# Optimization experiments

Measured on AMD Instinct MI355X. Metric: run time of the kernel, lower is better.

Reference implementation:

```python
import math
import jax, jax.numpy as jnp
import numpy as np

LAMBDA_TV = 0.005
LAMBDA_WAV = 0.005
MAX_ITER = 15
LEVELS = 3
TV_ITERS = 5  # prox_tv called with num_iter=5 in forward
S2 = math.sqrt(2.0)


def _fft2c(x):
    # x: (B, 2, H, W) real/imag channels -> centered 2D FFT, same layout
    xc = x[:, 0] + 1j * x[:, 1]
    kc = jnp.fft.fftshift(
        jnp.fft.fft2(jnp.fft.ifftshift(xc, axes=(-2, -1)), norm='ortho'),
        axes=(-2, -1))
    return jnp.stack([kc.real, kc.imag], axis=1)


def _ifft2c(x):
    xc = x[:, 0] + 1j * x[:, 1]
    ic = jnp.fft.fftshift(
        jnp.fft.ifft2(jnp.fft.ifftshift(xc, axes=(-2, -1)), norm='ortho'),
        axes=(-2, -1))
    return jnp.stack([ic.real, ic.imag], axis=1)


def _grad(x):
    # x: (N, 1, H, W) -> forward differences, (N, 2, H, W); last row/col zero
    dx = jnp.pad(x[:, :, :, 1:] - x[:, :, :, :-1], ((0, 0), (0, 0), (0, 0), (0, 1)))
    dy = jnp.pad(x[:, :, 1:, :] - x[:, :, :-1, :], ((0, 0), (0, 0), (0, 1), (0, 0)))
    return jnp.concatenate([dx, dy], axis=1)


def _div(p):
    # adjoint of _grad with the exact boundary handling of the torch code
    px, py = p[:, 0:1], p[:, 1:2]
    div_x = jnp.concatenate(
        [px[:, :, :, 0:1], px[:, :, :, 1:-1] - px[:, :, :, :-2], -px[:, :, :, -2:-1]],
        axis=-1)
    div_y = jnp.concatenate(
        [py[:, :, 0:1, :], py[:, :, 1:-1, :] - py[:, :, :-2, :], -py[:, :, -2:-1, :]],
        axis=2)
    return div_x + div_y


def _prox_tv(x, lam):
    # Chambolle dual iteration, applied per channel (vectorized over B*C)
    B, C, H, W = x.shape
    xc = x.reshape(B * C, 1, H, W)
    tau = 0.25

    def body(p, _):
        g = _grad(xc - lam * _div(p))
        pn = p + tau * g
        nrm = jnp.sqrt(jnp.sum(pn * pn, axis=1, keepdims=True) + 1e-8)
        return pn / jnp.maximum(nrm, 1.0), None

    p0 = jnp.zeros((B * C, 2, H, W), x.dtype)
    p, _ = jax.lax.scan(body, p0, None, length=TV_ITERS)
    return (xc - lam * _div(p)).reshape(B, C, H, W)


def _dwt2(x):
    x_lo = (x[:, :, :, ::2] + x[:, :, :, 1::2]) / S2
    x_hi = (x[:, :, :, ::2] - x[:, :, :, 1::2]) / S2
    ll = (x_lo[:, :, ::2] + x_lo[:, :, 1::2]) / S2
    lh = (x_lo[:, :, ::2] - x_lo[:, :, 1::2]) / S2
    hl = (x_hi[:, :, ::2] + x_hi[:, :, 1::2]) / S2
    hh = (x_hi[:, :, ::2] - x_hi[:, :, 1::2]) / S2
    return ll, (lh, hl, hh)


def _interleave(even, odd, axis):
    s = jnp.stack([even, odd], axis=axis + 1)
    shp = list(even.shape)
    shp[axis] *= 2
    return s.reshape(shp)


def _idwt2(ll, lh, hl, hh):
    x_lo = _interleave((ll + lh) / S2, (ll - lh) / S2, axis=2)  # rows
    x_hi = _interleave((hl + hh) / S2, (hl - hh) / S2, axis=2)
    return _interleave((x_lo + x_hi) / S2, (x_lo - x_hi) / S2, axis=3)  # cols


def _soft(x, t):
    return jnp.sign(x) * jnp.maximum(jnp.abs(x) - t, 0.0)


def setup_inputs() -> dict:
    key = jax.random.key(0)
    k1, k2 = jax.random.split(key)
    B, H, W = 16, 320, 320
    y = jax.random.normal(k1, (B, 2, H, W), jnp.float32)
    mask = (jax.random.uniform(k2, (B, 1, H, W)) < 0.3).astype(jnp.float32)
    return {"y": y, "mask": mask}


def reference(y, mask):
    def step(carry, _):
        x, z, t = carry
        # projected gradient for data fidelity (step_size = 1.0)
        g = _ifft2c(mask * (mask * _fft2c(z) - y))
        z_step = z - g
        # TV prox
        x_tv = _prox_tv(z_step, LAMBDA_TV)
        # wavelet decomposition + soft-threshold of detail subbands
        cur = x_tv
        details = []
        for _lvl in range(LEVELS):
            cur, d = _dwt2(cur)
            details.append(tuple(_soft(c, LAMBDA_WAV) for c in d))
        x_new = cur
        for d in reversed(details):
            x_new = _idwt2(x_new, *d)
        # FISTA momentum
        t_new = (1.0 + jnp.sqrt(1.0 + 4.0 * t * t)) / 2.0
        z_new = x_new + (t - 1.0) / t_new * (x_new - x)
        return (x_new, z_new, t_new), None

    x0 = _ifft2c(y)
    (x, _, _), _ = jax.lax.scan(jax.checkpoint(step), (x0, x0, jnp.float32(1.0)),
                                None, length=MAX_ITER)
    return x
```

## Files before the change

### kernel.cpp

```cpp
#include <hip/hip_runtime.h>
#include <math.h>

constexpr int WID  = 320;
constexpr int HWc  = 320 * 320;
constexpr int NIMG = 16;
constexpr int NSL  = 32;
constexpr int NTOT = NIMG * 2 * HWc;
constexpr float LAM_TV  = 0.005f;
constexpr float LAM_WAV = 0.005f;

__device__ __forceinline__ float softt(float v) {
    float a = fmaxf(fabsf(v) - LAM_WAV, 0.f);
    return copysignf(a, v);
}

struct Tw { float tc, ts; float stc[6], sts[6]; };

template<int SGN>
__device__ __forceinline__ Tw make_tw(int lane) {
    Tw tw;
    __sincosf((float)SGN * 6.283185307179586f * (float)lane / 320.f, &tw.ts, &tw.tc);
#pragma unroll
    for (int s = 0; s < 6; s++) {
        int h = 32 >> s;
        int j = lane & (h - 1);
        float ang = (float)SGN * 3.14159265358979323f * (float)j / (float)h;
        __sincosf(ang, &tw.sts[s], &tw.stc[s]);
    }
    return tw;
}

template<int SGN>
__device__ __forceinline__ void fft320_core(const float (&vr)[5], const float (&vi)[5],
                                            float (&Cr)[5], float (&Ci)[5],
                                            const Tw& tw, int lane) {
    const float cw1 = 0.30901699437494745f, sw1 = 0.9510565162951535f;
    const float cw2 = -0.8090169943749475f, sw2 = 0.5877852522924731f;
    const float cwt[5] = {1.f, cw1, cw2, cw2, cw1};
    const float swt[5] = {0.f, sw1, sw2, -sw2, -sw1};
    Cr[0] = vr[0] + vr[1] + vr[2] + vr[3] + vr[4];
    Ci[0] = vi[0] + vi[1] + vi[2] + vi[3] + vi[4];
#pragma unroll
    for (int k = 1; k < 5; k++) {
        float ar = vr[0], ai = vi[0];
#pragma unroll
        for (int m = 1; m < 5; m++) {
            int j = (m * k) % 5;
            float wr_ = cwt[j], wi_ = (float)SGN * swt[j];
            ar += vr[m] * wr_ - vi[m] * wi_;
            ai += vr[m] * wi_ + vi[m] * wr_;
        }
        Cr[k] = ar; Ci[k] = ai;
    }
    float twr = 1.f, twi = 0.f;
#pragma unroll
    for (int k = 1; k < 5; k++) {
        float nr = twr * tw.tc - twi * tw.ts;
        twi = twr * tw.ts + twi * tw.tc;
        twr = nr;
        float r = Cr[k] * twr - Ci[k] * twi;
        Ci[k]   = Cr[k] * twi + Ci[k] * twr;
        Cr[k]   = r;
    }
#pragma unroll
    for (int s = 0; s < 6; s++) {
        int h = 32 >> s;
        bool up = (lane & h) != 0;
#pragma unroll
        for (int k = 0; k < 5; k++) {
            float orr = __shfl_xor(Cr[k], h);
            float oii = __shfl_xor(Ci[k], h);
            if (up) {
                float dr = orr - Cr[k], di = oii - Ci[k];
                Cr[k] = dr * tw.stc[s] - di * tw.sts[s];
                Ci[k] = dr * tw.sts[s] + di * tw.stc[s];
            } else {
                Cr[k] += orr;
                Ci[k] += oii;
            }
        }
    }
}

template<int SGN, int EPI>
__global__ __launch_bounds__(256) void fft_row(const float* __restrict__ in,
                                               float* __restrict__ out,
                                               const float* __restrict__ aux1,
                                               float* __restrict__ out2) {
    const int lane = threadIdx.x & 63;
    const int wv   = threadIdx.x >> 6;
    const int L    = blockIdx.x * 4 + wv;
    const int img  = L / 320;
    const int l    = L - img * 320;
    const float* pre = in + (size_t)img * 2 * HWc + (size_t)l * WID;
    const float* pim = pre + HWc;

    float vr[5], vi[5];
    const float sgn_in = (lane & 1) ? -1.f : 1.f;
#pragma unroll
    for (int m = 0; m < 5; m++) {
        int n = lane + 64 * m;
        vr[m] = sgn_in * pre[n];
        vi[m] = sgn_in * pim[n];
    }
    Tw tw = make_tw<SGN>(lane);
    float Cr[5], Ci[5];
    fft320_core<SGN>(vr, vi, Cr, Ci, tw, lane);

    const int k1 = (int)(__brev((unsigned)lane) >> 26);
    float* qre = out + (size_t)img * 2 * HWc + (size_t)l * WID;
    float* qim = qre + HWc;
    const float scale = 0.05590169943749474f;
#pragma unroll
    for (int k = 0; k < 5; k++) {
        int kout = 5 * k1 + k;
        float s2 = (kout & 1) ? -scale : scale;
        float re = s2 * Cr[k];
        float im = s2 * Ci[k];
        const int idxs = kout + l * WID;
        if (EPI == 2) {
            re = aux1[(size_t)img * 2 * HWc + idxs] - re;
            im = aux1[(size_t)img * 2 * HWc + HWc + idxs] - im;
        }
        qre[kout] = re;
        qim[kout] = im;
        if (EPI == 3) {
            out2[(size_t)img * 2 * HWc + idxs]       = re;
            out2[(size_t)img * 2 * HWc + HWc + idxs] = im;
        }
    }
}

constexpr int CB   = 8;
constexpr int CPAD = CB + 1;

template<int SGN>
__device__ __forceinline__ void fft_line_lds(float (*tile)[320][CPAD], int cl,
                                             int lane, const Tw& tw) {
    float vr[5], vi[5], Cr[5], Ci[5];
    const float sgn_in = (lane & 1) ? -1.f : 1.f;
#pragma unroll
    for (int m = 0; m < 5; m++) {
        int n = lane + 64 * m;
        vr[m] = sgn_in * tile[0][n][cl];
        vi[m] = sgn_in * tile[1][n][cl];
    }
    fft320_core<SGN>(vr, vi, Cr, Ci, tw, lane);
    const int k1 = (int)(__brev((unsigned)lane) >> 26);
    const float scale = 0.05590169943749474f;
#pragma unroll
    for (int k = 0; k < 5; k++) {
        int kout = 5 * k1 + k;
        float s2 = (kout & 1) ? -scale : scale;
        tile[0][kout][cl] = s2 * Cr[k];
        tile[1][kout][cl] = s2 * Ci[k];
    }
}

template<int MODE>
__global__ __launch_bounds__(512) void fft_col(const float* __restrict__ in,
                                               float* __restrict__ out,
                                               const float* __restrict__ y,
                                               const float* __restrict__ mask) {
    __shared__ float tile[2][320][CPAD];
    const int tid = threadIdx.x;
    const int bpi = WID / CB;
    const int img = blockIdx.x / bpi;
    const int c0  = (blockIdx.x - img * bpi) * CB;
    const size_t ibase = (size_t)img * 2 * HWc;
    constexpr int C4 = CB / 4;
    constexpr int NE = 320 * C4;

#pragma unroll
    for (int comp = 0; comp < 2; comp++) {
        const float* p = in + ibase + (size_t)comp * HWc + c0;
        for (int i = tid; i < NE; i += 512) {
            int row = i >> 1, cg = (i & 1) << 2;
            float4 v = *(const float4*)(p + row * WID + cg);
            float* t = &tile[comp][row][cg];
            t[0] = v.x; t[1] = v.y; t[2] = v.z; t[3] = v.w;
        }
    }
    __syncthreads();

    const int lane = tid & 63;
    const int wv   = tid >> 6;

    if (MODE == 1) {
        Tw twf = make_tw<-1>(lane);
        fft_line_lds<-1>(tile, wv, lane, twf);
        __syncthreads();
        const float* pm  = mask + (size_t)img * HWc + c0;
        const float* pyr = y + ibase + c0;
        const float* pyi = y + ibase + HWc + c0;
        for (int i = tid; i < NE; i += 512) {
            int row = i >> 1, cg = (i & 1) << 2;
            float4 m4 = *(const float4*)(pm  + row * WID + cg);
            float4 yr = *(const float4*)(pyr + row * WID + cg);
            float4 yi = *(const float4*)(pyi + row * WID + cg);
            float* tr = &tile[0][row][cg];
            float* ti = &tile[1][row][cg];
            tr[0] = m4.x * (m4.x * tr[0] - yr.x);
            tr[1] = m4.y * (m4.y * tr[1] - yr.y);
            tr[2] = m4.z * (m4.z * tr[2] - yr.z);
            tr[3] = m4.w * (m4.w * tr[3] - yr.w);
            ti[0] = m4.x * (m4.x * ti[0] - yi.x);
            ti[1] = m4.y * (m4.y * ti[1] - yi.y);
            ti[2] = m4.z * (m4.z * ti[2] - yi.z);
            ti[3] = m4.w * (m4.w * ti[3] - yi.w);
        }
        __syncthreads();
    }
    {
        Tw twi = make_tw<1>(lane);
        fft_line_lds<1>(tile, wv, lane, twi);
    }
    __syncthreads();
#pragma unroll
    for (int comp = 0; comp < 2; comp++) {
        float* p = out + ibase + (size_t)comp * HWc + c0;
        for (int i = tid; i < NE; i += 512) {
            int row = i >> 1, cg = (i & 1) << 2;
            const float* t = &tile[comp][row][cg];
            *(float4*)(p + row * WID + cg) = make_float4(t[0], t[1], t[2], t[3]);
        }
    }
}

constexpr int TIR = 16;
constexpr int TVR = TIR + 10;
constexpr int TIC = 48;
constexpr int TCOLS = 7;
constexpr int TROWS = WID / TIR;
constexpr int TPS = TROWS * TCOLS;

template<bool EDGE>
__device__ __forceinline__ void tv_core(const float* __restrict__ g, int gi0, int gj,
                                        float (&uf)[TIR]) {
    float z_[TVR], px_[TVR], py_[TVR];
    const bool colin = !EDGE || ((unsigned)gj < (unsigned)WID);
#pragma unroll
    for (int r = 0; r < TVR; r++) {
        int gi = gi0 + r;
        float v = 0.f;
        if (!EDGE) {
            v = g[gi * WID + gj];
        } else {
            bool in = colin && ((unsigned)gi < (unsigned)WID);
            if (in) v = g[gi * WID + gj];
        }
        z_[r] = v; px_[r] = 0.f; py_[r] = 0.f;
    }
    const bool gj_le0 = EDGE && (gj <= 0);
    const bool gj_hi  = EDGE && (gj >= WID - 1);
    const bool gx_on  = !EDGE || (gj < WID - 1);

#pragma clang loop unroll(disable)
    for (int it = 0; it < 5; it++) {
        float ucur, unext;
        {
            float pxm = __shfl_up(px_[0], 1);
            float divx, divy;
            if (!EDGE) {
                divx = px_[0] - pxm;
                divy = 0.f;
            } else {
                int gi = gi0;
                divx = gj_le0 ? px_[0] : (gj_hi ? -pxm : px_[0] - pxm);
                divy = (gi <= 0) ? py_[0] : ((gi >= WID - 1) ? -py_[0] : 0.f);
            }
            ucur = z_[0] - LAM_TV * (divx + divy);
        }
#pragma unroll
        for (int r = 0; r < TVR - 1; r++) {
            {
                float pxm = __shfl_up(px_[r + 1], 1);
                float divx, divy;
                if (!EDGE) {
                    divx = px_[r + 1] - pxm;
                    divy = py_[r + 1] - py_[r];
                } else {
                    int gi1 = gi0 + r + 1;
                    divx = gj_le0 ? px_[r + 1] : (gj_hi ? -pxm : px_[r + 1] - pxm);
                    divy = (gi1 <= 0) ? py_[r + 1]
                         : ((gi1 >= WID - 1) ? -py_[r] : py_[r + 1] - py_[r]);
                }
                unext = z_[r + 1] - LAM_TV * (divx + divy);
            }
            {
                float un = __shfl_down(ucur, 1);
                float gx, gy;
                if (!EDGE) {
                    gx = un - ucur;
                    gy = unext - ucur;
                } else {
                    int gi = gi0 + r;
                    gx = gx_on ? un - ucur : 0.f;
                    gy = (gi < WID - 1) ? unext - ucur : 0.f;
                }
                float px = fmaf(0.25f, gx, px_[r]);
                float py = fmaf(0.25f, gy, py_[r]);
                float n2 = fmaf(px, px, fmaf(py, py, 1e-8f));
                float inv = fminf(rsqrtf(n2), 1.f);
                px_[r] = px * inv;
                py_[r] = py * inv;
            }
            ucur = unext;
        }
        {
            float un = __shfl_down(ucur, 1);
            float gx = gx_on ? un - ucur : 0.f;
            float px = fmaf(0.25f, gx, px_[TVR - 1]);
            float py = py_[TVR - 1];
            float n2 = fmaf(px, px, fmaf(py, py, 1e-8f));
            float inv = fminf(rsqrtf(n2), 1.f);
            px_[TVR - 1] = px * inv;
            py_[TVR - 1] = py * inv;
        }
    }
#pragma unroll
    for (int r = 5; r < TVR - 5; r++) {
        float pxm = __shfl_up(px_[r], 1);
        float divx, divy;
        if (!EDGE) {
            divx = px_[r] - pxm;
            divy = py_[r] - py_[r - 1];
        } else {
            int gi = gi0 + r;
            divx = gj_le0 ? px_[r] : (gj_hi ? -pxm : px_[r] - pxm);
            divy = (gi <= 0) ? py_[r]
                 : ((gi >= WID - 1) ? -py_[r - 1] : py_[r] - py_[r - 1]);
        }
        uf[r - 5] = z_[r] - LAM_TV * (divx + divy);
    }
}

__global__ __launch_bounds__(256, 4) void tv_wav_fista(const float* __restrict__ zs,
                                                       float* __restrict__ x,
                                                       float* __restrict__ z,
                                                       float beta) {
    const int lane = threadIdx.x & 63;
    const int wv   = __builtin_amdgcn_readfirstlane(threadIdx.x >> 6);
    const int w    = blockIdx.x * 4 + wv;
    const int sl   = w / TPS;
    const int rem  = w - sl * TPS;
    const int trow = rem / TCOLS;
    const int tcol = rem - trow * TCOLS;
    const int gi0  = trow * TIR - 5;
    const int gj   = tcol * TIC - 8 + lane;
    const float* g = zs + (size_t)sl * HWc;

    float uf[TIR];
    const bool interior = (trow >= 1) && (trow <= TROWS - 2) &&
                          (tcol >= 1) && (tcol <= TCOLS - 2);
    if (interior) tv_core<false>(g, gi0, gj, uf);
    else          tv_core<true >(g, gi0, gj, uf);

    const float sc1 = (lane & 1) ? -1.f : 1.f;
    const float sc2 = (lane & 2) ? -1.f : 1.f;
    const float sc3 = (lane & 4) ? -1.f : 1.f;

    float ll1[8], lh1[8], hl1[8], hh1[8];
#pragma unroll
    for (int k = 0; k < 8; k++) {
        float a0 = uf[2 * k], a1 = uf[2 * k + 1];
        float n0 = __shfl_xor(a0, 1), n1 = __shfl_xor(a1, 1);
        float h0 = a0 + n0, d0 = sc1 * (a0 - n0);
        float h1 = a1 + n1, d1 = sc1 * (a1 - n1);
        ll1[k] = (h0 + h1) * 0.5f;
        lh1[k] = softt((h0 - h1) * 0.5f);
        hl1[k] = softt((d0 + d1) * 0.5f);
        hh1[k] = softt((d0 - d1) * 0.5f);
    }
    float ll2[4], lh2[4], hl2[4], hh2[4];
#pragma unroll
    for (int k = 0; k < 4; k++) {
        float a0 = ll1[2 * k], a1 = ll1[2 * k + 1];
        float n0 = __shfl_xor(a0, 2), n1 = __shfl_xor(a1, 2);
        float h0 = a0 + n0, d0 = sc2 * (a0 - n0);
        float h1 = a1 + n1, d1 = sc2 * (a1 - n1);
        ll2[k] = (h0 + h1) * 0.5f;
        lh2[k] = softt((h0 - h1) * 0.5f);
        hl2[k] = softt((d0 + d1) * 0.5f);
        hh2[k] = softt((d0 - d1) * 0.5f);
    }
    float ll3[2], lh3[2], hl3[2], hh3[2];
#pragma unroll
    for (int k = 0; k < 2; k++) {
        float a0 = ll2[2 * k], a1 = ll2[2 * k + 1];
        float n0 = __shfl_xor(a0, 4), n1 = __shfl_xor(a1, 4);
        float h0 = a0 + n0, d0 = sc3 * (a0 - n0);
        float h1 = a1 + n1, d1 = sc3 * (a1 - n1);
        ll3[k] = (h0 + h1) * 0.5f;
        lh3[k] = softt((h0 - h1) * 0.5f);
        hl3[k] = softt((d0 + d1) * 0.5f);
        hh3[k] = softt((d0 - d1) * 0.5f);
    }
    float l2p[4];
#pragma unroll
    for (int k = 0; k < 2; k++) {
        l2p[2 * k]     = 0.5f * ((ll3[k] + lh3[k]) + sc3 * (hl3[k] + hh3[k]));
        l2p[2 * k + 1] = 0.5f * ((ll3[k] - lh3[k]) + sc3 * (hl3[k] - hh3[k]));
    }
    float l1p[8];
#pragma unroll
    for (int k = 0; k < 4; k++) {
        l1p[2 * k]     = 0.5f * ((l2p[k] + lh2[k]) + sc2 * (hl2[k] + hh2[k]));
        l1p[2 * k + 1] = 0.5f * ((l2p[k] - lh2[k]) + sc2 * (hl2[k] - hh2[k]));
    }
    float xn[TIR];
#pragma unroll
    for (int k = 0; k < 8; k++) {
        xn[2 * k]     = 0.5f * ((l1p[k] + lh1[k]) + sc1 * (hl1[k] + hh1[k]));
        xn[2 * k + 1] = 0.5f * ((l1p[k] - lh1[k]) + sc1 * (hl1[k] - hh1[k]));
    }

    const bool wcol = (lane >= 8) && (lane < 56) && ((unsigned)gj < (unsigned)WID);
    float* px = x + (size_t)sl * HWc;
    float* pz = z + (size_t)sl * HWc;
    const int gi_int0 = trow * TIR;
#pragma unroll
    for (int i = 0; i < TIR; i++) {
        int off = (gi_int0 + i) * WID + gj;
        float xo = wcol ? px[off] : 0.f;
        float zn = xn[i] + beta * (xn[i] - xo);
        if (wcol) {
            px[off] = xn[i];
            pz[off] = zn;
        }
    }
}

extern "C" void kernel_launch(void* const* d_in, const int* in_sizes, int n_in,
                              void* d_out, int out_size, void* d_ws, size_t ws_size,
                              hipStream_t stream) {
    const float* y    = (const float*)d_in[0];
    const float* mask = (const float*)d_in[1];
    float* x = (float*)d_out;

    float* ws = (float*)d_ws;
    float* z  = ws;
    float* t1 = ws + (size_t)NTOT;
    float* t2 = ws + 2 * (size_t)NTOT;

    const int ROW_BLKS = (NIMG * 320) / 4;
    const int COL_BLKS = NIMG * (WID / CB);
    const int TV_BLKS  = (NSL * TPS) / 4;

    fft_col<0><<<COL_BLKS, 512, 0, stream>>>(y, t1, nullptr, nullptr);
    fft_row<1, 3><<<ROW_BLKS, 256, 0, stream>>>(t1, x, nullptr, z);

    float t = 1.f;
    for (int it = 0; it < 15; it++) {
        fft_row<-1, 0><<<ROW_BLKS, 256, 0, stream>>>(z, t1, nullptr, nullptr);
        fft_col<1><<<COL_BLKS, 512, 0, stream>>>(t1, t2, y, mask);
        fft_row<1, 2><<<ROW_BLKS, 256, 0, stream>>>(t2, t1, z, nullptr);

        float tn   = (1.f + sqrtf(1.f + 4.f * t * t)) * 0.5f;
        float beta = (t - 1.f) / tn;
        t = tn;
        tv_wav_fista<<<TV_BLKS, 256, 0, stream>>>(t1, x, z, beta);
    }
    (void)in_sizes; (void)n_in; (void)out_size; (void)ws_size;
}
```

Before: 1.428 ms.

## Shrink TV tile height and halo, prefetch FFT epilogue operands

The fused TV/wavelet/FISTA kernel now processes 8-row tiles with a 4-row halo instead of 16 rows with a 5-row halo. This cuts per-thread register arrays and drops the forced occupancy hint from the launch bounds. In exchange, the share of redundant halo work per tile goes up. Separately, the row-FFT epilogue loads its subtraction operand before the FFT core runs, so that memory latency overlaps the compute.

```diff
diff --git a/kernel.cpp b/kernel.cpp
--- a/kernel.cpp
+++ b/kernel.cpp
@@ -92,8 +92,10 @@
     const int L    = blockIdx.x * 4 + wv;
     const int img  = L / 320;
     const int l    = L - img * 320;
-    const float* pre = in + (size_t)img * 2 * HWc + (size_t)l * WID;
+    const size_t ibase = (size_t)img * 2 * HWc;
+    const float* pre = in + ibase + (size_t)l * WID;
     const float* pim = pre + HWc;
+    const int k1 = (int)(__brev((unsigned)lane) >> 26);
 
     float vr[5], vi[5];
     const float sgn_in = (lane & 1) ? -1.f : 1.f;
@@ -103,12 +105,21 @@
         vr[m] = sgn_in * pre[n];
         vi[m] = sgn_in * pim[n];
     }
+    float zr[5], zi[5];
+    if (EPI == 2) {
+#pragma unroll
+        for (int k = 0; k < 5; k++) {
+            int idxs = 5 * k1 + k + l * WID;
+            zr[k] = aux1[ibase + idxs];
+            zi[k] = aux1[ibase + HWc + idxs];
+        }
+    }
+
     Tw tw = make_tw<SGN>(lane);
     float Cr[5], Ci[5];
     fft320_core<SGN>(vr, vi, Cr, Ci, tw, lane);
 
-    const int k1 = (int)(__brev((unsigned)lane) >> 26);
-    float* qre = out + (size_t)img * 2 * HWc + (size_t)l * WID;
+    float* qre = out + ibase + (size_t)l * WID;
     float* qim = qre + HWc;
     const float scale = 0.05590169943749474f;
 #pragma unroll
@@ -119,14 +130,14 @@
         float im = s2 * Ci[k];
         const int idxs = kout + l * WID;
         if (EPI == 2) {
-            re = aux1[(size_t)img * 2 * HWc + idxs] - re;
-            im = aux1[(size_t)img * 2 * HWc + HWc + idxs] - im;
+            re = zr[k] - re;
+            im = zi[k] - im;
         }
         qre[kout] = re;
         qim[kout] = im;
         if (EPI == 3) {
-            out2[(size_t)img * 2 * HWc + idxs]       = re;
-            out2[(size_t)img * 2 * HWc + HWc + idxs] = im;
+            out2[ibase + idxs]       = re;
+            out2[ibase + HWc + idxs] = im;
         }
     }
 }
@@ -227,8 +238,9 @@
     }
 }
 
-constexpr int TIR = 16;
-constexpr int TVR = TIR + 10;
+constexpr int HALO = 4;
+constexpr int TIR = 8;
+constexpr int TVR = TIR + 2 * HALO;
 constexpr int TIC = 48;
 constexpr int TCOLS = 7;
 constexpr int TROWS = WID / TIR;
@@ -319,7 +331,7 @@
         }
     }
 #pragma unroll
-    for (int r = 5; r < TVR - 5; r++) {
+    for (int r = HALO; r < TVR - HALO; r++) {
         float pxm = __shfl_up(px_[r], 1);
         float divx, divy;
         if (!EDGE) {
@@ -331,14 +343,14 @@
             divy = (gi <= 0) ? py_[r]
                  : ((gi >= WID - 1) ? -py_[r - 1] : py_[r] - py_[r - 1]);
         }
-        uf[r - 5] = z_[r] - LAM_TV * (divx + divy);
-    }
-}
-
-__global__ __launch_bounds__(256, 4) void tv_wav_fista(const float* __restrict__ zs,
-                                                       float* __restrict__ x,
-                                                       float* __restrict__ z,
-                                                       float beta) {
+        uf[r - HALO] = z_[r] - LAM_TV * (divx + divy);
+    }
+}
+
+__global__ __launch_bounds__(256) void tv_wav_fista(const float* __restrict__ zs,
+                                                    float* __restrict__ x,
+                                                    float* __restrict__ z,
+                                                    float beta) {
     const int lane = threadIdx.x & 63;
     const int wv   = __builtin_amdgcn_readfirstlane(threadIdx.x >> 6);
     const int w    = blockIdx.x * 4 + wv;
@@ -346,7 +358,7 @@
     const int rem  = w - sl * TPS;
     const int trow = rem / TCOLS;
     const int tcol = rem - trow * TCOLS;
-    const int gi0  = trow * TIR - 5;
+    const int gi0  = trow * TIR - HALO;
     const int gj   = tcol * TIC - 8 + lane;
     const float* g = zs + (size_t)sl * HWc;
 
@@ -360,9 +372,9 @@
     const float sc2 = (lane & 2) ? -1.f : 1.f;
     const float sc3 = (lane & 4) ? -1.f : 1.f;
 
-    float ll1[8], lh1[8], hl1[8], hh1[8];
-#pragma unroll
-    for (int k = 0; k < 8; k++) {
+    float ll1[4], lh1[4], hl1[4], hh1[4];
+#pragma unroll
+    for (int k = 0; k < 4; k++) {
         float a0 = uf[2 * k], a1 = uf[2 * k + 1];
         float n0 = __shfl_xor(a0, 1), n1 = __shfl_xor(a1, 1);
         float h0 = a0 + n0, d0 = sc1 * (a0 - n0);
@@ -372,9 +384,9 @@
         hl1[k] = softt((d0 + d1) * 0.5f);
         hh1[k] = softt((d0 - d1) * 0.5f);
     }
-    float ll2[4], lh2[4], hl2[4], hh2[4];
-#pragma unroll
-    for (int k = 0; k < 4; k++) {
+    float ll2[2], lh2[2], hl2[2], hh2[2];
+#pragma unroll
+    for (int k = 0; k < 2; k++) {
         float a0 = ll1[2 * k], a1 = ll1[2 * k + 1];
         float n0 = __shfl_xor(a0, 2), n1 = __shfl_xor(a1, 2);
         float h0 = a0 + n0, d0 = sc2 * (a0 - n0);
@@ -384,33 +396,29 @@
         hl2[k] = softt((d0 + d1) * 0.5f);
         hh2[k] = softt((d0 - d1) * 0.5f);
     }
-    float ll3[2], lh3[2], hl3[2], hh3[2];
-#pragma unroll
-    for (int k = 0; k < 2; k++) {
-        float a0 = ll2[2 * k], a1 = ll2[2 * k + 1];
+    float ll3, lh3, hl3, hh3;
+    {
+        float a0 = ll2[0], a1 = ll2[1];
         float n0 = __shfl_xor(a0, 4), n1 = __shfl_xor(a1, 4);
         float h0 = a0 + n0, d0 = sc3 * (a0 - n0);
         float h1 = a1 + n1, d1 = sc3 * (a1 - n1);
-        ll3[k] = (h0 + h1) * 0.5f;
-        lh3[k] = softt((h0 - h1) * 0.5f);
-        hl3[k] = softt((d0 + d1) * 0.5f);
-        hh3[k] = softt((d0 - d1) * 0.5f);
-    }
-    float l2p[4];
+        ll3 = (h0 + h1) * 0.5f;
+        lh3 = softt((h0 - h1) * 0.5f);
+        hl3 = softt((d0 + d1) * 0.5f);
+        hh3 = softt((d0 - d1) * 0.5f);
+    }
+    float l2p[2];
+    l2p[0] = 0.5f * ((ll3 + lh3) + sc3 * (hl3 + hh3));
+    l2p[1] = 0.5f * ((ll3 - lh3) + sc3 * (hl3 - hh3));
+    float l1p[4];
 #pragma unroll
     for (int k = 0; k < 2; k++) {
-        l2p[2 * k]     = 0.5f * ((ll3[k] + lh3[k]) + sc3 * (hl3[k] + hh3[k]));
-        l2p[2 * k + 1] = 0.5f * ((ll3[k] - lh3[k]) + sc3 * (hl3[k] - hh3[k]));
-    }
-    float l1p[8];
-#pragma unroll
-    for (int k = 0; k < 4; k++) {
         l1p[2 * k]     = 0.5f * ((l2p[k] + lh2[k]) + sc2 * (hl2[k] + hh2[k]));
         l1p[2 * k + 1] = 0.5f * ((l2p[k] - lh2[k]) + sc2 * (hl2[k] - hh2[k]));
     }
     float xn[TIR];
 #pragma unroll
-    for (int k = 0; k < 8; k++) {
+    for (int k = 0; k < 4; k++) {
         xn[2 * k]     = 0.5f * ((l1p[k] + lh1[k]) + sc1 * (hl1[k] + hh1[k]));
         xn[2 * k + 1] = 0.5f * ((l1p[k] - lh1[k]) + sc1 * (hl1[k] - hh1[k]));
     }
```

Result: faster. 1.337 ms (-6.3%).
